# Optimization experiments

Hardware: AMD Instinct MI355X
Metric: run time of the kernel (lower is better)

## Reference

```python
import jax, jax.numpy as jnp
import numpy as np

EMBED = 768
HEADS = 12
HEAD_DIM = EMBED // HEADS  # 64
NUM_CLS = 1
WIN = 16        # one-sided window radius
DIL = 4         # dilation
THETA = 10000.0
COORD_HIGH = 100000.0


def _rotate_half(x):
    # [..., x1, x2, ...] -> [..., -x2, x1, ...] over adjacent pairs
    x1 = x[..., 0::2]
    x2 = x[..., 1::2]
    return jnp.stack([-x2, x1], axis=-1).reshape(x.shape)


def _rope2d(x, coords):
    # x: (B, H, L, head_dim); coords: (B, L, 2) pixel coords
    half = HEAD_DIM // 2
    inv_freq = 1.0 / THETA ** (jnp.arange(0, half, 2, dtype=jnp.float32) / half)  # (half/2,)
    xy = coords.astype(jnp.float32) / COORD_HIGH
    fx = xy[..., 0:1] * inv_freq  # (B, L, half/2)
    fy = xy[..., 1:2] * inv_freq
    fx = jnp.repeat(fx, 2, axis=-1)  # (B, L, half)
    fy = jnp.repeat(fy, 2, axis=-1)
    freqs = jnp.concatenate([fx, fy], axis=-1)  # (B, L, head_dim)
    cos = jnp.cos(freqs)[:, None]  # (B, 1, L, head_dim)
    sin = jnp.sin(freqs)[:, None]
    return x * cos + _rotate_half(x) * sin


def setup_inputs() -> dict:
    key = jax.random.key(0)
    ks = jax.random.split(key, 5)
    B, L = 1, 4096
    S = L + NUM_CLS
    x = jax.random.normal(ks[0], (B, S, EMBED), jnp.float32)
    coords = jax.random.randint(ks[1], (B, L, 2), 0, 100000).astype(jnp.int32)
    qkv_w = jax.random.normal(ks[2], (3 * EMBED, EMBED), jnp.float32) * 0.02
    qkv_b = jnp.zeros((3 * EMBED,), jnp.float32)
    out_w = jax.random.normal(ks[3], (EMBED, EMBED), jnp.float32) * 0.02
    out_b = jnp.zeros((EMBED,), jnp.float32)
    return {"x": x, "coords": coords, "qkv_w": qkv_w, "qkv_b": qkv_b,
            "out_w": out_w, "out_b": out_b}


def reference(x, coords, qkv_w, qkv_b, out_w, out_b):
    B, S, E = x.shape
    L = S - NUM_CLS
    # QKV projection -> (3, B, H, S, hd)
    qkv = (x @ qkv_w.T + qkv_b).reshape(B, S, 3, HEADS, HEAD_DIM)
    qkv = qkv.transpose(2, 0, 3, 1, 4)
    q, k, v = qkv[0], qkv[1], qkv[2]
    # 2D RoPE on patch tokens only
    q = jnp.concatenate([q[:, :, :NUM_CLS], _rope2d(q[:, :, NUM_CLS:], coords)], axis=2)
    k = jnp.concatenate([k[:, :, :NUM_CLS], _rope2d(k[:, :, NUM_CLS:], coords)], axis=2)
    scale = 1.0 / np.sqrt(HEAD_DIM).astype(np.float32)

    q_cls, k_cls, v_cls = q[:, :, :NUM_CLS], k[:, :, :NUM_CLS], v[:, :, :NUM_CLS]
    q_p, k_p, v_p = q[:, :, NUM_CLS:], k[:, :, NUM_CLS:], v[:, :, NUM_CLS:]

    # CLS (global) queries attend to everything
    cls_scores = jnp.einsum('bhqd,bhkd->bhqk', q_cls, k) * scale
    cls_out = jnp.einsum('bhqk,bhkd->bhqd', jax.nn.softmax(cls_scores, axis=-1), v)

    # Patch queries: single softmax over [CLS keys | dilated local window]
    win_len = 2 * WIN + 1
    pos = jnp.arange(L)
    rel = (jnp.arange(win_len) - WIN) * DIL
    key_idx = pos[:, None] + rel[None, :]          # (L, W) absolute patch key index
    valid = (key_idx >= 0) & (key_idx < L)         # boundary patches: masked, not wrapped
    gidx = jnp.clip(key_idx, 0, L - 1)
    k_win = jnp.take(k_p, gidx, axis=2)            # (B, H, L, W, hd)
    v_win = jnp.take(v_p, gidx, axis=2)
    s_win = jnp.einsum('bhld,bhlwd->bhlw', q_p, k_win) * scale
    s_win = jnp.where(valid[None, None], s_win, -jnp.inf)
    s_cls = jnp.einsum('bhld,bhcd->bhlc', q_p, k_cls) * scale
    attn = jax.nn.softmax(jnp.concatenate([s_cls, s_win], axis=-1), axis=-1)
    a_cls, a_win = attn[..., :NUM_CLS], attn[..., NUM_CLS:]
    patch_out = (jnp.einsum('bhlc,bhcd->bhld', a_cls, v_cls)
                 + jnp.einsum('bhlw,bhlwd->bhld', a_win, v_win))

    out = jnp.concatenate([cls_out, patch_out], axis=2)   # (B, H, S, hd)
    out = out.transpose(0, 2, 1, 3).reshape(B, S, E)
    return out @ out_w.T + out_b
```

## Files before the change

### kernel.cpp

```cpp
#include <hip/hip_runtime.h>
#include <hip/hip_bf16.h>

namespace {

constexpr int kS = 4097;
constexpr int kL = 4096;
constexpr int kE = 768;
constexpr int kH = 12;
constexpr int kD = 64;
constexpr int kQKVN = 2304;
constexpr int kT = 1024;
constexpr int kClsChunks = 32;
constexpr int kClsStride = 68;
constexpr float kScale = 0.125f;

typedef short short8 __attribute__((ext_vector_type(8)));
typedef short short4v __attribute__((ext_vector_type(4)));
typedef float f32x4 __attribute__((ext_vector_type(4)));

__device__ inline short f2bf(float x) {
  __hip_bfloat16 b = __float2bfloat16(x);
  return *reinterpret_cast<short*>(&b);
}
__device__ inline float bf2f(short u) {
  unsigned int x = ((unsigned int)(unsigned short)u) << 16;
  union { unsigned int u32; float f; } c;
  c.u32 = x;
  return c.f;
}

__device__ inline void store_c(float* p, float v) { *p = v; }
__device__ inline void store_c(short* p, float v) { *p = f2bf(v); }

__device__ inline int xcd_swz(int bid, int nwg) {
  const int q = nwg >> 3, r = nwg & 7;
  const int x = bid & 7, o = bid >> 3;
  return (x < r ? x * (q + 1) : r * (q + 1) + (x - r) * q) + o;
}

__global__ __launch_bounds__(256) void cvt3_kernel(const float* __restrict__ x,
                                                   const float* __restrict__ w,
                                                   const float* __restrict__ ow,
                                                   short* __restrict__ xb,
                                                   short* __restrict__ wb,
                                                   short* __restrict__ owb,
                                                   int n4x, int n4w, int n4o) {
  const int total = n4x + n4w + n4o;
  int i = blockIdx.x * blockDim.x + threadIdx.x;
  const int stride = gridDim.x * blockDim.x;
  for (; i < total; i += stride) {
    const float* src;
    short* dst;
    int k;
    if (i < n4x) { src = x; dst = xb; k = i; }
    else if (i < n4x + n4w) { src = w; dst = wb; k = i - n4x; }
    else { src = ow; dst = owb; k = i - n4x - n4w; }
    f32x4 v = reinterpret_cast<const f32x4*>(src)[k];
    short4v o;
#pragma unroll
    for (int j = 0; j < 4; ++j) o[j] = f2bf(v[j]);
    reinterpret_cast<short4v*>(dst)[k] = o;
  }
}

template <bool ROPE, typename TC>
__global__ __launch_bounds__(256) void gemm_tile_kernel(const short* __restrict__ A,
                                                        const short* __restrict__ W,
                                                        const float* __restrict__ bias,
                                                        TC* __restrict__ C,
                                                        int Mreal, int N, int K, int ntm,
                                                        const int* __restrict__ coords) {
  __shared__ short Ash[2][128 * 32];
  __shared__ short Bsh[2][128 * 32];
  const int nwg = gridDim.x;
  const int wid = xcd_swz(blockIdx.x, nwg);
  const int m0 = (wid % ntm) * 128;
  const int n0 = (wid / ntm) * 128;
  const int t = threadIdx.x;
  const int lane = t & 63;
  const int wave = t >> 6;
  const int wr = wave >> 1, wc = wave & 1;
  const int lrow = lane & 15;
  const int kg = (lane >> 4) << 3;

  const int srow = t >> 2;
  const int scol = (t & 3) << 3;
  int arow0 = m0 + srow;       if (arow0 > Mreal - 1) arow0 = Mreal - 1;
  int arow1 = m0 + 64 + srow;  if (arow1 > Mreal - 1) arow1 = Mreal - 1;
  const int brow0 = n0 + srow;
  const int brow1 = n0 + 64 + srow;

  const short* pa0 = A + (size_t)arow0 * K + scol;
  const short* pa1 = A + (size_t)arow1 * K + scol;
  const short* pb0 = W + (size_t)brow0 * K + scol;
  const short* pb1 = W + (size_t)brow1 * K + scol;

  f32x4 acc[4][4] = {};
  const int nsteps = K / 32;

  short8 rA0 = *reinterpret_cast<const short8*>(pa0);
  short8 rA1 = *reinterpret_cast<const short8*>(pa1);
  short8 rB0 = *reinterpret_cast<const short8*>(pb0);
  short8 rB1 = *reinterpret_cast<const short8*>(pb1);
  *reinterpret_cast<short8*>(&Ash[0][t * 8]) = rA0;
  *reinterpret_cast<short8*>(&Ash[0][2048 + t * 8]) = rA1;
  *reinterpret_cast<short8*>(&Bsh[0][t * 8]) = rB0;
  *reinterpret_cast<short8*>(&Bsh[0][2048 + t * 8]) = rB1;
  asm volatile("s_waitcnt lgkmcnt(0)" ::: "memory");
  __builtin_amdgcn_s_barrier();
  __builtin_amdgcn_sched_barrier(0);

  int cur = 0;
  for (int tt = 0; tt < nsteps; ++tt) {
    if (tt + 1 < nsteps) {
      const int k1 = (tt + 1) * 32;
      rA0 = *reinterpret_cast<const short8*>(pa0 + k1);
      rA1 = *reinterpret_cast<const short8*>(pa1 + k1);
      rB0 = *reinterpret_cast<const short8*>(pb0 + k1);
      rB1 = *reinterpret_cast<const short8*>(pb1 + k1);
    }

    short8 a[4], b[4];
#pragma unroll
    for (int mi = 0; mi < 4; ++mi)
      a[mi] = *reinterpret_cast<const short8*>(&Ash[cur][(wr * 64 + mi * 16 + lrow) * 32 + kg]);
#pragma unroll
    for (int ni = 0; ni < 4; ++ni)
      b[ni] = *reinterpret_cast<const short8*>(&Bsh[cur][(wc * 64 + ni * 16 + lrow) * 32 + kg]);
#pragma unroll
    for (int mi = 0; mi < 4; ++mi)
#pragma unroll
      for (int ni = 0; ni < 4; ++ni)
        acc[mi][ni] = __builtin_amdgcn_mfma_f32_16x16x32_bf16(a[mi], b[ni], acc[mi][ni], 0, 0, 0);

    __builtin_amdgcn_s_barrier();
    __builtin_amdgcn_sched_barrier(0);

    if (tt + 1 < nsteps) {
      *reinterpret_cast<short8*>(&Ash[cur ^ 1][t * 8]) = rA0;
      *reinterpret_cast<short8*>(&Ash[cur ^ 1][2048 + t * 8]) = rA1;
      *reinterpret_cast<short8*>(&Bsh[cur ^ 1][t * 8]) = rB0;
      *reinterpret_cast<short8*>(&Bsh[cur ^ 1][2048 + t * 8]) = rB1;
    }
    asm volatile("s_waitcnt lgkmcnt(0)" ::: "memory");
    __builtin_amdgcn_sched_barrier(0);
    __builtin_amdgcn_s_barrier();
    __builtin_amdgcn_sched_barrier(0);
    cur ^= 1;
  }

  const int rg = (lane >> 4) << 2;
  for (int ni = 0; ni < 4; ++ni) {
    const int col = n0 + wc * 64 + ni * 16 + lrow;
    const float bz = bias[col];
    const int sec = col / 768;
    const int dh = col & 63;
    const bool odd = dh & 1;
    const int jf = (dh >> 1) & 15;
    const bool usex = (dh >> 1) < 16;
    const float invf = __powf(10000.0f, -(float)jf * (1.0f / 16.0f));
    for (int mi = 0; mi < 4; ++mi) {
      const int rowb = m0 + wr * 64 + mi * 16 + rg;
#pragma unroll
      for (int r = 0; r < 4; ++r) {
        const int row = rowb + r;
        float v = acc[mi][ni][r] + bz;
        if (ROPE && sec != 2) {
          const float partner = __shfl_xor(v, 1);
          float cs = 1.f, sn = 0.f;
          if (row > 0) {
            const int cl = min(row, kS - 1) - 1;
            const float cx = (float)coords[cl * 2] * 1e-5f;
            const float cy = (float)coords[cl * 2 + 1] * 1e-5f;
            __sincosf((usex ? cx : cy) * invf, &sn, &cs);
          }
          v = odd ? (v * cs + partner * sn) : (v * cs - partner * sn);
          if (sec == 0) v *= kScale;
        }
        if (row < Mreal) store_c(&C[(size_t)row * N + col], v);
      }
    }
  }
}

__global__ __launch_bounds__(256) void attn_kernel(const short* __restrict__ qkv,
                                                   short* __restrict__ attn,
                                                   float* __restrict__ part) {
  __shared__ short Pl[4][32][104];
  __shared__ float sm[4], sl[4], sa[4][64];
  const int lane = threadIdx.x & 63;
  const int wv = threadIdx.x >> 6;

  if (blockIdx.x >= 384) {
    const int idx = blockIdx.x - 384;
    const int h = idx >> 5;
    const int c = idx & 31;
    const int start = c * 128;
    const int end = (c == kClsChunks - 1) ? kS : start + 128;
    const float qd = bf2f(qkv[h * kD + lane]);
    float m = -INFINITY, lsum = 0.f, acc = 0.f;
    for (int s = start + wv; s < end; s += 4) {
      float tt = qd * bf2f(qkv[(size_t)s * kQKVN + kE + h * kD + lane]);
      tt += __shfl_xor(tt, 1); tt += __shfl_xor(tt, 2); tt += __shfl_xor(tt, 4);
      tt += __shfl_xor(tt, 8); tt += __shfl_xor(tt, 16); tt += __shfl_xor(tt, 32);
      const float vd = bf2f(qkv[(size_t)s * kQKVN + 2 * kE + h * kD + lane]);
      const float mnew = fmaxf(m, tt);
      const float cor = __expf(m - mnew);
      const float p = __expf(tt - mnew);
      lsum = lsum * cor + p;
      acc = acc * cor + p * vd;
      m = mnew;
    }
    sa[wv][lane] = acc;
    if (lane == 0) { sm[wv] = m; sl[wv] = lsum; }
    __syncthreads();
    if (wv == 0) {
      float M = fmaxf(fmaxf(sm[0], sm[1]), fmaxf(sm[2], sm[3]));
      float Lt = 0.f, Av = 0.f;
#pragma unroll
      for (int w = 0; w < 4; ++w) {
        const float cw = __expf(sm[w] - M);
        Lt += sl[w] * cw;
        Av += sa[w][lane] * cw;
      }
      float* p = part + ((size_t)h * kClsChunks + c) * kClsStride;
      p[lane] = Av;
      if (lane == 0) { p[64] = M; p[65] = Lt; }
    }
    return;
  }

  const int unit = blockIdx.x * 4 + wv;
  const int t0 = (unit & 31) * 32;
  const int res = (unit >> 5) & 3;
  const int h = unit >> 7;
  const int lrow = lane & 15;
  const int lgrp = lane >> 4;
  const int kg = lgrp * 8;
  const int rg = lgrp * 4;

  f32x4 s_acc[2][4] = {};
  f32x4 s_cls[2] = {};
  short8 aq[2][2];
#pragma unroll
  for (int mi = 0; mi < 2; ++mi) {
    const int tq = t0 + mi * 16 + lrow;
    const size_t row = (size_t)(4 * tq + res + 1) * kQKVN + h * kD;
#pragma unroll
    for (int ks = 0; ks < 2; ++ks)
      aq[mi][ks] = *reinterpret_cast<const short8*>(qkv + row + ks * 32 + kg);
  }
#pragma unroll
  for (int ni = 0; ni < 4; ++ni) {
    int u = t0 - 16 + ni * 16 + lrow;
    u = min(max(u, 0), kT - 1);
    const size_t row = (size_t)(4 * u + res + 1) * kQKVN + kE + h * kD;
    short8 bk[2];
#pragma unroll
    for (int ks = 0; ks < 2; ++ks)
      bk[ks] = *reinterpret_cast<const short8*>(qkv + row + ks * 32 + kg);
#pragma unroll
    for (int mi = 0; mi < 2; ++mi)
#pragma unroll
      for (int ks = 0; ks < 2; ++ks)
        s_acc[mi][ni] = __builtin_amdgcn_mfma_f32_16x16x32_bf16(aq[mi][ks], bk[ks], s_acc[mi][ni], 0, 0, 0);
  }
  {
    short8 bc[2] = {};
    if (lrow == 0) {
#pragma unroll
      for (int ks = 0; ks < 2; ++ks)
        bc[ks] = *reinterpret_cast<const short8*>(qkv + kE + h * kD + ks * 32 + kg);
    }
#pragma unroll
    for (int mi = 0; mi < 2; ++mi)
#pragma unroll
      for (int ks = 0; ks < 2; ++ks)
        s_cls[mi] = __builtin_amdgcn_mfma_f32_16x16x32_bf16(aq[mi][ks], bc[ks], s_cls[mi], 0, 0, 0);
  }

#pragma unroll
  for (int i = 0; i < 2; ++i) {
    const int idx = i * 64 + lane;
    const int q = idx >> 2, ch = idx & 3;
    short8 z = {};
    *reinterpret_cast<short8*>(&Pl[wv][q][64 + ch * 8]) = z;
  }

#pragma unroll
  for (int mi = 0; mi < 2; ++mi) {
#pragma unroll
    for (int r = 0; r < 4; ++r) {
      const int q = mi * 16 + rg + r;
      float sw[4];
      float m = -INFINITY;
#pragma unroll
      for (int ni = 0; ni < 4; ++ni) {
        const int kk = ni * 16 + lrow;
        const int u = t0 - 16 + kk;
        const bool valid = (kk >= q) & (kk <= q + 32) & (u >= 0) & (u < kT);
        sw[ni] = valid ? s_acc[mi][ni][r] : -INFINITY;
        m = fmaxf(m, sw[ni]);
      }
      float scl = (lrow == 0) ? s_cls[mi][r] : -INFINITY;
      m = fmaxf(m, scl);
      m = fmaxf(m, __shfl_xor(m, 1)); m = fmaxf(m, __shfl_xor(m, 2));
      m = fmaxf(m, __shfl_xor(m, 4)); m = fmaxf(m, __shfl_xor(m, 8));
      float lsum = 0.f, ps[4];
#pragma unroll
      for (int ni = 0; ni < 4; ++ni) { ps[ni] = __expf(sw[ni] - m); lsum += ps[ni]; }
      const float pc = __expf(scl - m);
      lsum += pc;
      lsum += __shfl_xor(lsum, 1); lsum += __shfl_xor(lsum, 2);
      lsum += __shfl_xor(lsum, 4); lsum += __shfl_xor(lsum, 8);
      const float inv = __builtin_amdgcn_rcpf(lsum);
#pragma unroll
      for (int ni = 0; ni < 4; ++ni) Pl[wv][q][ni * 16 + lrow] = f2bf(ps[ni] * inv);
      if (lrow == 0) Pl[wv][q][64] = f2bf(pc * inv);
    }
  }

  f32x4 o_acc[4][2] = {};
#pragma unroll
  for (int ks = 0; ks < 3; ++ks) {
    short8 bp[2];
#pragma unroll
    for (int nq = 0; nq < 2; ++nq)
      bp[nq] = *reinterpret_cast<const short8*>(&Pl[wv][nq * 16 + lrow][ks * 32 + kg]);
    short8 av[4];
#pragma unroll
    for (int md = 0; md < 4; ++md) {
      if (ks < 2) {
        const int d = md * 16 + lrow;
#pragma unroll
        for (int e = 0; e < 8; ++e) {
          const int kk = ks * 32 + kg + e;
          int u = t0 - 16 + kk;
          u = min(max(u, 0), kT - 1);
          av[md][e] = qkv[(size_t)(4 * u + res + 1) * kQKVN + 2 * kE + h * kD + d];
        }
      } else {
        short8 z = {};
        av[md] = z;
        if (lgrp == 0)
          av[md][0] = qkv[2 * kE + h * kD + md * 16 + lrow];
      }
#pragma unroll
      for (int nq = 0; nq < 2; ++nq)
        o_acc[md][nq] = __builtin_amdgcn_mfma_f32_16x16x32_bf16(av[md], bp[nq], o_acc[md][nq], 0, 0, 0);
    }
  }

#pragma unroll
  for (int md = 0; md < 4; ++md)
#pragma unroll
    for (int nq = 0; nq < 2; ++nq)
#pragma unroll
      for (int r = 0; r < 4; ++r) {
        const int d = md * 16 + rg + r;
        const int q = nq * 16 + lrow;
        const int s = 4 * (t0 + q) + res + 1;
        attn[(size_t)s * kE + h * kD + d] = f2bf(o_acc[md][nq][r]);
      }
}

__global__ __launch_bounds__(64) void cls_combine_kernel(const float* __restrict__ part,
                                                         short* __restrict__ attn) {
  const int h = blockIdx.x;
  const int lane = threadIdx.x;
  float mc[kClsChunks], lc[kClsChunks], ac[kClsChunks];
#pragma unroll
  for (int c = 0; c < kClsChunks; ++c) {
    const float* p = part + ((size_t)h * kClsChunks + c) * kClsStride;
    mc[c] = p[64];
    lc[c] = p[65];
    ac[c] = p[lane];
  }
  float M = -INFINITY;
#pragma unroll
  for (int c = 0; c < kClsChunks; ++c) M = fmaxf(M, mc[c]);
  float L = 0.f, A = 0.f;
#pragma unroll
  for (int c = 0; c < kClsChunks; ++c) {
    const float w = __expf(mc[c] - M);
    L += lc[c] * w;
    A += ac[c] * w;
  }
  attn[h * kD + lane] = f2bf(A / L);
}

}

extern "C" void kernel_launch(void* const* d_in, const int* in_sizes, int n_in,
                              void* d_out, int out_size, void* d_ws, size_t ws_size,
                              hipStream_t stream) {
  const float* x = (const float*)d_in[0];
  const int* coords = (const int*)d_in[1];
  const float* qkv_w = (const float*)d_in[2];
  const float* qkv_b = (const float*)d_in[3];
  const float* out_w = (const float*)d_in[4];
  const float* out_b = (const float*)d_in[5];
  float* out = (float*)d_out;

  char* p = (char*)d_ws;
  short* qkvb = (short*)p;                p += (size_t)kS * kQKVN * sizeof(short);
  short* xb = (short*)p;                  p += (size_t)kS * kE * sizeof(short);
  short* wb = (short*)p;                  p += (size_t)kQKVN * kE * sizeof(short);
  short* owb = (short*)p;                 p += (size_t)kE * kE * sizeof(short);
  short* attnb = (short*)p;               p += (size_t)kS * kE * sizeof(short);
  float* clsp = (float*)p;

  const int n4x = kS * kE / 4;
  const int n4w = kQKVN * kE / 4;
  const int n4o = kE * kE / 4;
  cvt3_kernel<<<2048, 256, 0, stream>>>(x, qkv_w, out_w, xb, wb, owb, n4x, n4w, n4o);

  gemm_tile_kernel<true, short><<<594, 256, 0, stream>>>(xb, wb, qkv_b, qkvb, kS, kQKVN, kE, 33, coords);
  attn_kernel<<<768, 256, 0, stream>>>(qkvb, attnb, clsp);
  cls_combine_kernel<<<kH, 64, 0, stream>>>(clsp, attnb);
  gemm_tile_kernel<false, float><<<198, 256, 0, stream>>>(attnb, owb, out_b, out, kS, kE, kE, 33, nullptr);
}
```

Baseline: 102.0 us.

## Pad GEMM LDS tiles and deepen global-load prefetch with one barrier per step

```diff
diff --git a/kernel.cpp b/kernel.cpp
--- a/kernel.cpp
+++ b/kernel.cpp
@@ -12,6 +12,7 @@
 constexpr int kT = 1024;
 constexpr int kClsChunks = 32;
 constexpr int kClsStride = 68;
+constexpr int kP = 40;
 constexpr float kScale = 0.125f;
 
 typedef short short8 __attribute__((ext_vector_type(8)));
@@ -70,8 +71,8 @@
                                                         TC* __restrict__ C,
                                                         int Mreal, int N, int K, int ntm,
                                                         const int* __restrict__ coords) {
-  __shared__ short Ash[2][128 * 32];
-  __shared__ short Bsh[2][128 * 32];
+  __shared__ short Ash[2][128 * kP];
+  __shared__ short Bsh[2][128 * kP];
   const int nwg = gridDim.x;
   const int wid = xcd_swz(blockIdx.x, nwg);
   const int m0 = (wid % ntm) * 128;
@@ -95,59 +96,75 @@
   const short* pb0 = W + (size_t)brow0 * K + scol;
   const short* pb1 = W + (size_t)brow1 * K + scol;
 
+  const int w0 = srow * kP + scol;
+  const int w1 = (64 + srow) * kP + scol;
+
+#define LOAD4(ra0, ra1, rb0, rb1, k)                         \
+  do {                                                       \
+    ra0 = *reinterpret_cast<const short8*>(pa0 + (k));       \
+    ra1 = *reinterpret_cast<const short8*>(pa1 + (k));       \
+    rb0 = *reinterpret_cast<const short8*>(pb0 + (k));       \
+    rb1 = *reinterpret_cast<const short8*>(pb1 + (k));       \
+  } while (0)
+
+#define WRITE4(buf, ra0, ra1, rb0, rb1)                      \
+  do {                                                       \
+    *reinterpret_cast<short8*>(&Ash[buf][w0]) = ra0;         \
+    *reinterpret_cast<short8*>(&Ash[buf][w1]) = ra1;         \
+    *reinterpret_cast<short8*>(&Bsh[buf][w0]) = rb0;         \
+    *reinterpret_cast<short8*>(&Bsh[buf][w1]) = rb1;         \
+  } while (0)
+
+#define COMPUTE(buf)                                                                   \
+  do {                                                                                 \
+    short8 a[4], b[4];                                                                 \
+    _Pragma("unroll") for (int mi = 0; mi < 4; ++mi)                                   \
+        a[mi] = *reinterpret_cast<const short8*>(                                      \
+            &Ash[buf][(wr * 64 + mi * 16 + lrow) * kP + kg]);                          \
+    _Pragma("unroll") for (int ni = 0; ni < 4; ++ni)                                   \
+        b[ni] = *reinterpret_cast<const short8*>(                                      \
+            &Bsh[buf][(wc * 64 + ni * 16 + lrow) * kP + kg]);                          \
+    _Pragma("unroll") for (int mi = 0; mi < 4; ++mi)                                   \
+        _Pragma("unroll") for (int ni = 0; ni < 4; ++ni)                               \
+            acc[mi][ni] =                                                              \
+                __builtin_amdgcn_mfma_f32_16x16x32_bf16(a[mi], b[ni], acc[mi][ni], 0, 0, 0); \
+  } while (0)
+
+#define ENDSTEP                                              \
+  do {                                                       \
+    asm volatile("s_waitcnt lgkmcnt(0)" ::: "memory");       \
+    __builtin_amdgcn_sched_barrier(0);                       \
+    __builtin_amdgcn_s_barrier();                            \
+    __builtin_amdgcn_sched_barrier(0);                       \
+  } while (0)
+
   f32x4 acc[4][4] = {};
   const int nsteps = K / 32;
 
-  short8 rA0 = *reinterpret_cast<const short8*>(pa0);
-  short8 rA1 = *reinterpret_cast<const short8*>(pa1);
-  short8 rB0 = *reinterpret_cast<const short8*>(pb0);
-  short8 rB1 = *reinterpret_cast<const short8*>(pb1);
-  *reinterpret_cast<short8*>(&Ash[0][t * 8]) = rA0;
-  *reinterpret_cast<short8*>(&Ash[0][2048 + t * 8]) = rA1;
-  *reinterpret_cast<short8*>(&Bsh[0][t * 8]) = rB0;
-  *reinterpret_cast<short8*>(&Bsh[0][2048 + t * 8]) = rB1;
-  asm volatile("s_waitcnt lgkmcnt(0)" ::: "memory");
-  __builtin_amdgcn_s_barrier();
-  __builtin_amdgcn_sched_barrier(0);
-
-  int cur = 0;
-  for (int tt = 0; tt < nsteps; ++tt) {
-    if (tt + 1 < nsteps) {
-      const int k1 = (tt + 1) * 32;
-      rA0 = *reinterpret_cast<const short8*>(pa0 + k1);
-      rA1 = *reinterpret_cast<const short8*>(pa1 + k1);
-      rB0 = *reinterpret_cast<const short8*>(pb0 + k1);
-      rB1 = *reinterpret_cast<const short8*>(pb1 + k1);
-    }
-
-    short8 a[4], b[4];
-#pragma unroll
-    for (int mi = 0; mi < 4; ++mi)
-      a[mi] = *reinterpret_cast<const short8*>(&Ash[cur][(wr * 64 + mi * 16 + lrow) * 32 + kg]);
-#pragma unroll
-    for (int ni = 0; ni < 4; ++ni)
-      b[ni] = *reinterpret_cast<const short8*>(&Bsh[cur][(wc * 64 + ni * 16 + lrow) * 32 + kg]);
-#pragma unroll
-    for (int mi = 0; mi < 4; ++mi)
-#pragma unroll
-      for (int ni = 0; ni < 4; ++ni)
-        acc[mi][ni] = __builtin_amdgcn_mfma_f32_16x16x32_bf16(a[mi], b[ni], acc[mi][ni], 0, 0, 0);
-
-    __builtin_amdgcn_s_barrier();
-    __builtin_amdgcn_sched_barrier(0);
-
-    if (tt + 1 < nsteps) {
-      *reinterpret_cast<short8*>(&Ash[cur ^ 1][t * 8]) = rA0;
-      *reinterpret_cast<short8*>(&Ash[cur ^ 1][2048 + t * 8]) = rA1;
-      *reinterpret_cast<short8*>(&Bsh[cur ^ 1][t * 8]) = rB0;
-      *reinterpret_cast<short8*>(&Bsh[cur ^ 1][2048 + t * 8]) = rB1;
-    }
-    asm volatile("s_waitcnt lgkmcnt(0)" ::: "memory");
-    __builtin_amdgcn_sched_barrier(0);
-    __builtin_amdgcn_s_barrier();
-    __builtin_amdgcn_sched_barrier(0);
-    cur ^= 1;
-  }
+  short8 sA0, sA1, sB0, sB1;
+  short8 tA0, tA1, tB0, tB1;
+
+  LOAD4(sA0, sA1, sB0, sB1, 0);
+  WRITE4(0, sA0, sA1, sB0, sB1);
+  LOAD4(tA0, tA1, tB0, tB1, 32);
+  ENDSTEP;
+
+  for (int tt = 0; tt < nsteps; tt += 2) {
+    if (tt + 2 < nsteps) LOAD4(sA0, sA1, sB0, sB1, (tt + 2) * 32);
+    COMPUTE(0);
+    WRITE4(1, tA0, tA1, tB0, tB1);
+    ENDSTEP;
+    if (tt + 3 < nsteps) LOAD4(tA0, tA1, tB0, tB1, (tt + 3) * 32);
+    COMPUTE(1);
+    if (tt + 2 < nsteps) {
+      WRITE4(0, sA0, sA1, sB0, sB1);
+      ENDSTEP;
+    }
+  }
+#undef LOAD4
+#undef WRITE4
+#undef COMPUTE
+#undef ENDSTEP
 
   const int rg = (lane >> 4) << 2;
   for (int ni = 0; ni < 4; ++ni) {
```

Result: slower. 128.6 us (+26.1%).

## Fuse x fp32-to-bf16 conversion into QKV GEMM and load B tiles directly to LDS

Applied to the files above, without the earlier changes.

```diff
diff --git a/kernel.cpp b/kernel.cpp
--- a/kernel.cpp
+++ b/kernel.cpp
@@ -38,23 +38,57 @@
   return (x < r ? x * (q + 1) : r * (q + 1) + (x - r) * q) + o;
 }
 
-__global__ __launch_bounds__(256) void cvt3_kernel(const float* __restrict__ x,
-                                                   const float* __restrict__ w,
+#define GLOAD_LDS16(g, l)                                                        \
+  __builtin_amdgcn_global_load_lds(                                              \
+      (const __attribute__((address_space(1))) unsigned int*)(g),                \
+      (__attribute__((address_space(3))) unsigned int*)(l), 16, 0, 0)
+
+template <typename AT> struct ARegs;
+template <> struct ARegs<float> {
+  f32x4 a0lo, a0hi, a1lo, a1hi;
+  __device__ inline void load(const float* __restrict__ p0, const float* __restrict__ p1) {
+    a0lo = *reinterpret_cast<const f32x4*>(p0);
+    a0hi = *reinterpret_cast<const f32x4*>(p0 + 4);
+    a1lo = *reinterpret_cast<const f32x4*>(p1);
+    a1hi = *reinterpret_cast<const f32x4*>(p1 + 4);
+  }
+  __device__ inline void write(short* d0, short* d1) const {
+    short8 w0, w1;
+#pragma unroll
+    for (int j = 0; j < 4; ++j) {
+      w0[j] = f2bf(a0lo[j]); w0[j + 4] = f2bf(a0hi[j]);
+      w1[j] = f2bf(a1lo[j]); w1[j + 4] = f2bf(a1hi[j]);
+    }
+    *reinterpret_cast<short8*>(d0) = w0;
+    *reinterpret_cast<short8*>(d1) = w1;
+  }
+};
+template <> struct ARegs<short> {
+  short8 a0, a1;
+  __device__ inline void load(const short* __restrict__ p0, const short* __restrict__ p1) {
+    a0 = *reinterpret_cast<const short8*>(p0);
+    a1 = *reinterpret_cast<const short8*>(p1);
+  }
+  __device__ inline void write(short* d0, short* d1) const {
+    *reinterpret_cast<short8*>(d0) = a0;
+    *reinterpret_cast<short8*>(d1) = a1;
+  }
+};
+
+__global__ __launch_bounds__(256) void cvtw_kernel(const float* __restrict__ w,
                                                    const float* __restrict__ ow,
-                                                   short* __restrict__ xb,
                                                    short* __restrict__ wb,
                                                    short* __restrict__ owb,
-                                                   int n4x, int n4w, int n4o) {
-  const int total = n4x + n4w + n4o;
+                                                   int n4w, int n4o) {
+  const int total = n4w + n4o;
   int i = blockIdx.x * blockDim.x + threadIdx.x;
   const int stride = gridDim.x * blockDim.x;
   for (; i < total; i += stride) {
     const float* src;
     short* dst;
     int k;
-    if (i < n4x) { src = x; dst = xb; k = i; }
-    else if (i < n4x + n4w) { src = w; dst = wb; k = i - n4x; }
-    else { src = ow; dst = owb; k = i - n4x - n4w; }
+    if (i < n4w) { src = w; dst = wb; k = i; }
+    else { src = ow; dst = owb; k = i - n4w; }
     f32x4 v = reinterpret_cast<const f32x4*>(src)[k];
     short4v o;
 #pragma unroll
@@ -63,8 +97,8 @@
   }
 }
 
-template <bool ROPE, typename TC>
-__global__ __launch_bounds__(256) void gemm_tile_kernel(const short* __restrict__ A,
+template <bool ROPE, typename AT, typename TC>
+__global__ __launch_bounds__(256) void gemm_tile_kernel(const AT* __restrict__ A,
                                                         const short* __restrict__ W,
                                                         const float* __restrict__ bias,
                                                         TC* __restrict__ C,
@@ -90,34 +124,28 @@
   const int brow0 = n0 + srow;
   const int brow1 = n0 + 64 + srow;
 
-  const short* pa0 = A + (size_t)arow0 * K + scol;
-  const short* pa1 = A + (size_t)arow1 * K + scol;
+  const AT* pa0 = A + (size_t)arow0 * K + scol;
+  const AT* pa1 = A + (size_t)arow1 * K + scol;
   const short* pb0 = W + (size_t)brow0 * K + scol;
   const short* pb1 = W + (size_t)brow1 * K + scol;
 
+  ARegs<AT> ar;
   f32x4 acc[4][4] = {};
   const int nsteps = K / 32;
 
-  short8 rA0 = *reinterpret_cast<const short8*>(pa0);
-  short8 rA1 = *reinterpret_cast<const short8*>(pa1);
-  short8 rB0 = *reinterpret_cast<const short8*>(pb0);
-  short8 rB1 = *reinterpret_cast<const short8*>(pb1);
-  *reinterpret_cast<short8*>(&Ash[0][t * 8]) = rA0;
-  *reinterpret_cast<short8*>(&Ash[0][2048 + t * 8]) = rA1;
-  *reinterpret_cast<short8*>(&Bsh[0][t * 8]) = rB0;
-  *reinterpret_cast<short8*>(&Bsh[0][2048 + t * 8]) = rB1;
-  asm volatile("s_waitcnt lgkmcnt(0)" ::: "memory");
-  __builtin_amdgcn_s_barrier();
-  __builtin_amdgcn_sched_barrier(0);
+  ar.load(pa0, pa1);
+  GLOAD_LDS16(pb0, &Bsh[0][t * 8]);
+  GLOAD_LDS16(pb1, &Bsh[0][2048 + t * 8]);
+  ar.write(&Ash[0][t * 8], &Ash[0][2048 + t * 8]);
+  __syncthreads();
 
   int cur = 0;
   for (int tt = 0; tt < nsteps; ++tt) {
     if (tt + 1 < nsteps) {
       const int k1 = (tt + 1) * 32;
-      rA0 = *reinterpret_cast<const short8*>(pa0 + k1);
-      rA1 = *reinterpret_cast<const short8*>(pa1 + k1);
-      rB0 = *reinterpret_cast<const short8*>(pb0 + k1);
-      rB1 = *reinterpret_cast<const short8*>(pb1 + k1);
+      ar.load(pa0 + k1, pa1 + k1);
+      GLOAD_LDS16(pb0 + k1, &Bsh[cur ^ 1][t * 8]);
+      GLOAD_LDS16(pb1 + k1, &Bsh[cur ^ 1][2048 + t * 8]);
     }
 
     short8 a[4], b[4];
@@ -133,19 +161,9 @@
       for (int ni = 0; ni < 4; ++ni)
         acc[mi][ni] = __builtin_amdgcn_mfma_f32_16x16x32_bf16(a[mi], b[ni], acc[mi][ni], 0, 0, 0);
 
-    __builtin_amdgcn_s_barrier();
-    __builtin_amdgcn_sched_barrier(0);
-
-    if (tt + 1 < nsteps) {
-      *reinterpret_cast<short8*>(&Ash[cur ^ 1][t * 8]) = rA0;
-      *reinterpret_cast<short8*>(&Ash[cur ^ 1][2048 + t * 8]) = rA1;
-      *reinterpret_cast<short8*>(&Bsh[cur ^ 1][t * 8]) = rB0;
-      *reinterpret_cast<short8*>(&Bsh[cur ^ 1][2048 + t * 8]) = rB1;
-    }
-    asm volatile("s_waitcnt lgkmcnt(0)" ::: "memory");
-    __builtin_amdgcn_sched_barrier(0);
-    __builtin_amdgcn_s_barrier();
-    __builtin_amdgcn_sched_barrier(0);
+    if (tt + 1 < nsteps)
+      ar.write(&Ash[cur ^ 1][t * 8], &Ash[cur ^ 1][2048 + t * 8]);
+    __syncthreads();
     cur ^= 1;
   }
 
@@ -404,19 +422,17 @@
 
   char* p = (char*)d_ws;
   short* qkvb = (short*)p;                p += (size_t)kS * kQKVN * sizeof(short);
-  short* xb = (short*)p;                  p += (size_t)kS * kE * sizeof(short);
   short* wb = (short*)p;                  p += (size_t)kQKVN * kE * sizeof(short);
   short* owb = (short*)p;                 p += (size_t)kE * kE * sizeof(short);
   short* attnb = (short*)p;               p += (size_t)kS * kE * sizeof(short);
   float* clsp = (float*)p;
 
-  const int n4x = kS * kE / 4;
   const int n4w = kQKVN * kE / 4;
   const int n4o = kE * kE / 4;
-  cvt3_kernel<<<2048, 256, 0, stream>>>(x, qkv_w, out_w, xb, wb, owb, n4x, n4w, n4o);
-
-  gemm_tile_kernel<true, short><<<594, 256, 0, stream>>>(xb, wb, qkv_b, qkvb, kS, kQKVN, kE, 33, coords);
+  cvtw_kernel<<<2048, 256, 0, stream>>>(qkv_w, out_w, wb, owb, n4w, n4o);
+
+  gemm_tile_kernel<true, float, short><<<594, 256, 0, stream>>>(x, wb, qkv_b, qkvb, kS, kQKVN, kE, 33, coords);
   attn_kernel<<<768, 256, 0, stream>>>(qkvb, attnb, clsp);
   cls_combine_kernel<<<kH, 64, 0, stream>>>(clsp, attnb);
-  gemm_tile_kernel<false, float><<<198, 256, 0, stream>>>(attnb, owb, out_b, out, kS, kE, kE, 33, nullptr);
-}
+  gemm_tile_kernel<false, short, float><<<198, 256, 0, stream>>>(attnb, owb, out_b, out, kS, kE, kE, 33, nullptr);
+}
```

Measured after the change: 108.7 us. 6.6% more time.
